# Kernel tuning notes

Measured on AMD Instinct MI355X. Metric: run time of the kernel, lower is better.

The kernel has to match this reference:

```python
import jax, jax.numpy as jnp
import numpy as np

D_MODEL = 1024
N_HEADS = 16
N_GROUPS = 4
HEAD_DIM = D_MODEL // N_HEADS          # 64
HPG = N_HEADS // N_GROUPS              # heads per group = 4
KV_DIM = N_GROUPS * HEAD_DIM           # 256


def setup_inputs() -> dict:
    key = jax.random.key(0)
    ks = jax.random.split(key, 9)
    B, T = 2, 2048
    s = 0.02
    return {
        "x":  jax.random.normal(ks[0], (B, T, D_MODEL), dtype=jnp.float32),
        "Wq": jax.random.normal(ks[1], (D_MODEL, D_MODEL), dtype=jnp.float32) * s,
        "bq": jnp.zeros((D_MODEL,), dtype=jnp.float32),
        "Wk": jax.random.normal(ks[2], (D_MODEL, KV_DIM), dtype=jnp.float32) * s,
        "bk": jnp.zeros((KV_DIM,), dtype=jnp.float32),
        "Wv": jax.random.normal(ks[3], (D_MODEL, KV_DIM), dtype=jnp.float32) * s,
        "bv": jnp.zeros((KV_DIM,), dtype=jnp.float32),
        "Wo": jax.random.normal(ks[4], (D_MODEL, D_MODEL), dtype=jnp.float32) * s,
        "bo": jnp.zeros((D_MODEL,), dtype=jnp.float32),
    }


def reference(x, Wq, bq, Wk, bk, Wv, bv, Wo, bo):
    B, T, C = x.shape
    q = x @ Wq + bq                                   # [B,T,C]
    k = x @ Wk + bk                                   # [B,T,G*hd]
    v = x @ Wv + bv

    # [B, G, hpg, T, hd] for q; [B, G, T, hd] for k,v (native GQA head sharing,
    # equivalent to repeat_interleave on the group dim in the torch code)
    q = q.reshape(B, T, N_GROUPS, HPG, HEAD_DIM).transpose(0, 2, 3, 1, 4)
    k = k.reshape(B, T, N_GROUPS, HEAD_DIM).transpose(0, 2, 1, 3)
    v = v.reshape(B, T, N_GROUPS, HEAD_DIM).transpose(0, 2, 1, 3)

    scale = 1.0 / jnp.sqrt(jnp.float32(HEAD_DIM))
    attn = jnp.einsum('bghqd,bgkd->bghqk', q, k) * scale   # [B,G,hpg,T,T]

    causal = jnp.tril(jnp.ones((T, T), dtype=bool))        # True = keep
    attn = jnp.where(causal, attn, jnp.float32(-jnp.inf))
    attn = jax.nn.softmax(attn, axis=-1)
    # dropout p=0.1 only in training mode; reference is eval mode (identity)

    out = jnp.einsum('bghqk,bgkd->bghqd', attn, v)         # [B,G,hpg,T,hd]
    out = out.transpose(0, 3, 1, 2, 4).reshape(B, T, C)
    return out @ Wo + bo
```

## Files before the change

### kernel.cpp

```cpp
#include <hip/hip_runtime.h>
#include <hip/hip_bf16.h>
#include <stdint.h>

#define D_MODEL 1024
#define T_LEN   2048
#define BATCH   2
#define N_HEADS 16
#define KV_DIM  256
#define QKV_N   1536
#define M_ROWS  (BATCH * T_LEN)

typedef unsigned short u16;
typedef __bf16 bf16x8 __attribute__((ext_vector_type(8)));
typedef __bf16 bf16x2 __attribute__((ext_vector_type(2)));
typedef float  f32x4  __attribute__((ext_vector_type(4)));

__device__ __forceinline__ u16 f2b(float f) {
    uint32_t u = __builtin_bit_cast(uint32_t, f);
    u += 0x7FFFu + ((u >> 16) & 1u);
    return (u16)(u >> 16);
}

__device__ __forceinline__ uint32_t pk_bf16(float a, float b) {
#if __has_builtin(__builtin_amdgcn_cvt_pk_bf16_f32)
    bf16x2 v = __builtin_amdgcn_cvt_pk_bf16_f32(a, b);
    return __builtin_bit_cast(uint32_t, v);
#else
    return (uint32_t)f2b(a) | ((uint32_t)f2b(b) << 16);
#endif
}

__device__ __forceinline__ void gl_lds16(const void* g, void* l) {
    __builtin_amdgcn_global_load_lds(g, l, 16, 0, 0);
}

__global__ __launch_bounds__(256) void prep(
    const float* __restrict__ x,
    const float* __restrict__ Wq, const float* __restrict__ Wk,
    const float* __restrict__ Wv, const float* __restrict__ Wo,
    u16* __restrict__ xb, u16* __restrict__ WcatT, u16* __restrict__ WoT)
{
    __shared__ u16 tile[32][33];
    int id = blockIdx.x;
    int tid = threadIdx.x;
    if (id < 2048) {
        int i = (id * 256 + tid) * 8;
        float4 a = *(const float4*)&x[i];
        float4 c = *(const float4*)&x[i + 4];
        u16 r[8] = { f2b(a.x), f2b(a.y), f2b(a.z), f2b(a.w),
                     f2b(c.x), f2b(c.y), f2b(c.z), f2b(c.w) };
        *(uint4*)&xb[i] = *(const uint4*)r;
        return;
    }
    int t = id - 2048;
    int bx = t % 80;
    int k0 = (t / 80) * 32;
    const float* src; u16* dst; int N, n0;
    if (bx < 32)       { src = Wq; dst = WcatT;                   N = 1024; n0 = bx * 32; }
    else if (bx < 40)  { src = Wk; dst = WcatT + 1024 * 1024;     N = 256;  n0 = (bx - 32) * 32; }
    else if (bx < 48)  { src = Wv; dst = WcatT + 1280 * 1024;     N = 256;  n0 = (bx - 40) * 32; }
    else               { src = Wo; dst = WoT;                     N = 1024; n0 = (bx - 48) * 32; }
    for (int i = 0; i < 4; ++i) {
        int idx = tid + i * 256;
        int r = idx >> 5, c = idx & 31;
        tile[r][c] = f2b(src[(size_t)(k0 + r) * N + (n0 + c)]);
    }
    __syncthreads();
    for (int i = 0; i < 4; ++i) {
        int idx = tid + i * 256;
        int r = idx >> 5, c = idx & 31;
        dst[(size_t)(n0 + r) * 1024 + (k0 + c)] = tile[c][r];
    }
}

__global__ __launch_bounds__(256) void gemm_qkv(
    const u16* __restrict__ A, const u16* __restrict__ BT,
    const float* __restrict__ bq, const float* __restrict__ bk,
    const float* __restrict__ bv, u16* __restrict__ Qb,
    u16* __restrict__ Kpack, u16* __restrict__ Vpack)
{
    constexpr int K = 1024;
    constexpr float SCALE = 0.125f * 1.44269504088896f;
    __shared__ __align__(16) u16 As[128 * 64];
    __shared__ __align__(16) u16 Bs[128 * 64];

    int tid  = threadIdx.x;
    int lane = tid & 63, w = tid >> 6;
    int quad = lane >> 4, l15 = lane & 15;
    int wr = w >> 1, wc = w & 1;
    int m0 = blockIdx.y * 128, n0 = blockIdx.x * 128;
    int lr = lane >> 3, lc = (lane & 7) * 8;

    f32x4 acc[4][4] = {};

    for (int k0 = 0; k0 < K; k0 += 64) {
        for (int t = 0; t < 4; ++t) {
            int rb = t * 32 + w * 8;
            gl_lds16(&A[(size_t)(m0 + rb + lr) * K + k0 + lc], &As[rb * 64]);
            gl_lds16(&BT[(size_t)(n0 + rb + lr) * K + k0 + lc], &Bs[rb * 64]);
        }
        __syncthreads();
        for (int kk = 0; kk < 64; kk += 32) {
            bf16x8 a[4], b[4];
            for (int i = 0; i < 4; ++i)
                a[i] = *(const bf16x8*)&As[(wr * 64 + i * 16 + l15) * 64 + kk + quad * 8];
            for (int j = 0; j < 4; ++j)
                b[j] = *(const bf16x8*)&Bs[(wc * 64 + j * 16 + l15) * 64 + kk + quad * 8];
            for (int i = 0; i < 4; ++i)
                for (int j = 0; j < 4; ++j)
                    acc[i][j] = __builtin_amdgcn_mfma_f32_16x16x32_bf16(
                        a[i], b[j], acc[i][j], 0, 0, 0);
        }
        __syncthreads();
    }

    for (int j = 0; j < 4; ++j) {
        int col = n0 + wc * 64 + j * 16 + l15;
        float bj = (col < 1024) ? bq[col] : (col < 1280) ? bk[col - 1024] : bv[col - 1280];
        for (int i = 0; i < 4; ++i) {
            int rowb = m0 + wr * 64 + i * 16 + quad * 4;
            int bb = rowb >> 11, keyloc = rowb & 2047;
            int t64 = keyloc >> 6;
            if (col < 1024) {
                for (int r = 0; r < 4; ++r)
                    Qb[(size_t)(rowb + r) * 1024 + col] =
                        f2b((acc[i][j][r] + bj) * SCALE);
            } else if (col < 1280) {
                int d = col - 1024; int g = d >> 6; d &= 63;
                int kk = d >> 5, qd = (d >> 3) & 3, e = d & 7;
                int ntk = (keyloc >> 4) & 3, l15k = keyloc & 15;
                size_t base = ((((size_t)(bb * 4 + g) * 32 + t64) * 2 + kk) * 4
                               + ntk) * 512 + qd * 128 + l15k * 8 + e;
                for (int r = 0; r < 4; ++r)
                    Kpack[base + r * 8] = f2b(acc[i][j][r] + bj);
            } else {
                int d = col - 1280; int g = d >> 6; d &= 63;
                int dt = d >> 4, l15v = d & 15;
                int kkp = (keyloc >> 5) & 1, qv = (keyloc >> 3) & 3, e0 = keyloc & 7;
                u16 tmp[4];
                for (int r = 0; r < 4; ++r) tmp[r] = f2b(acc[i][j][r] + bj);
                size_t base = ((((size_t)(bb * 4 + g) * 32 + t64) * 2 + kkp) * 4
                               + dt) * 512 + (qv * 16 + l15v) * 8 + e0;
                *(uint64_t*)&Vpack[base] = *(const uint64_t*)tmp;
            }
        }
    }
}

__global__ __launch_bounds__(256) void gemm_out(
    const u16* __restrict__ A, const u16* __restrict__ BT,
    const float* __restrict__ bias, float* __restrict__ C)
{
    constexpr int K = 1024, N = 1024;
    __shared__ __align__(16) u16 As[128 * 64];
    __shared__ __align__(16) u16 Bs[128 * 64];

    int tid  = threadIdx.x;
    int lane = tid & 63, w = tid >> 6;
    int quad = lane >> 4, l15 = lane & 15;
    int wr = w >> 1, wc = w & 1;
    int m0 = blockIdx.y * 128, n0 = blockIdx.x * 128;
    int lr = lane >> 3, lc = (lane & 7) * 8;

    f32x4 acc[4][4] = {};

    for (int k0 = 0; k0 < K; k0 += 64) {
        for (int t = 0; t < 4; ++t) {
            int rb = t * 32 + w * 8;
            gl_lds16(&A[(size_t)(m0 + rb + lr) * K + k0 + lc], &As[rb * 64]);
            gl_lds16(&BT[(size_t)(n0 + rb + lr) * K + k0 + lc], &Bs[rb * 64]);
        }
        __syncthreads();
        for (int kk = 0; kk < 64; kk += 32) {
            bf16x8 a[4], b[4];
            for (int i = 0; i < 4; ++i)
                a[i] = *(const bf16x8*)&As[(wr * 64 + i * 16 + l15) * 64 + kk + quad * 8];
            for (int j = 0; j < 4; ++j)
                b[j] = *(const bf16x8*)&Bs[(wc * 64 + j * 16 + l15) * 64 + kk + quad * 8];
            for (int i = 0; i < 4; ++i)
                for (int j = 0; j < 4; ++j)
                    acc[i][j] = __builtin_amdgcn_mfma_f32_16x16x32_bf16(
                        a[i], b[j], acc[i][j], 0, 0, 0);
        }
        __syncthreads();
    }

    for (int j = 0; j < 4; ++j) {
        int col = n0 + wc * 64 + j * 16 + l15;
        float bj = bias[col];
        for (int i = 0; i < 4; ++i) {
            int rowb = m0 + wr * 64 + i * 16 + quad * 4;
            for (int r = 0; r < 4; ++r)
                C[(size_t)(rowb + r) * N + col] = acc[i][j][r] + bj;
        }
    }
}

__global__ __launch_bounds__(256, 4) void attn_kernel(
    const u16* __restrict__ Qb,
    const u16* __restrict__ Kpack,
    const u16* __restrict__ Vpack,
    u16* __restrict__ AO)
{
    constexpr int LDP = 72;
    __shared__ __align__(16) u16 Ps[4][16 * LDP];

    int tid  = threadIdx.x;
    int lane = tid & 63, w = tid >> 6;
    int quad = lane >> 4, l15 = lane & 15;

    int gid = blockIdx.x;
    int b = gid & 1, g = (gid >> 1) & 3;
    int s = gid >> 3;
    int kq = s >> 5, tq = s & 31;
    int q4 = (kq & 1) ? tq : (31 - tq);
    int j  = q4 * 4 + kq;
    int head = g * 4 + w;
    int q0 = j * 16;
    int iters = q4 + 1;

    const u16* Qp = Qb + ((size_t)b * T_LEN + q0) * 1024 + head * 64;
    const u16* Kp = Kpack + (size_t)(b * 4 + g) * 131072 + (size_t)lane * 8;
    const u16* Vp = Vpack + (size_t)(b * 4 + g) * 131072 + (size_t)lane * 8;
    u16*       Op = AO + ((size_t)b * T_LEN + q0) * D_MODEL + head * 64;
    u16* Pw = Ps[w];

    bf16x8 Qfrag[2];
    #pragma unroll
    for (int kk = 0; kk < 2; ++kk)
        Qfrag[kk] = *(const bf16x8*)&Qp[(size_t)l15 * 1024 + kk * 32 + quad * 8];

    f32x4 o[4] = {};
    float lsum = 0.f;

    for (int tg = 0; tg < iters; ++tg) {
        bool diag = (tg == iters - 1);

        const u16* kb = Kp + (size_t)tg * 4096;
        bf16x8 aK[2][4];
        #pragma unroll
        for (int kk = 0; kk < 2; ++kk)
            #pragma unroll
            for (int ntk = 0; ntk < 4; ++ntk)
                aK[kk][ntk] = *(const bf16x8*)(kb + (kk * 4 + ntk) * 512);

        f32x4 sacc[4] = {};
        #pragma unroll
        for (int kk = 0; kk < 2; ++kk) {
            bf16x8 bQ = Qfrag[kk];
            #pragma unroll
            for (int ntk = 0; ntk < 4; ++ntk)
                sacc[ntk] = __builtin_amdgcn_mfma_f32_16x16x32_bf16(
                    aK[kk][ntk], bQ, sacc[ntk], 0, 0, 0);
        }
        int qrow = q0 + l15;
        float lacc = 0.f;
        #pragma unroll
        for (int ntk = 0; ntk < 4; ++ntk) {
            float p0, p1, p2, p3;
            if (diag) {
                int key = tg * 64 + ntk * 16 + quad * 4;
                p0 = (key + 0 <= qrow) ? exp2f(sacc[ntk][0]) : 0.f;
                p1 = (key + 1 <= qrow) ? exp2f(sacc[ntk][1]) : 0.f;
                p2 = (key + 2 <= qrow) ? exp2f(sacc[ntk][2]) : 0.f;
                p3 = (key + 3 <= qrow) ? exp2f(sacc[ntk][3]) : 0.f;
            } else {
                p0 = exp2f(sacc[ntk][0]);
                p1 = exp2f(sacc[ntk][1]);
                p2 = exp2f(sacc[ntk][2]);
                p3 = exp2f(sacc[ntk][3]);
            }
            lacc += (p0 + p1) + (p2 + p3);
            uint2 pv;
            pv.x = pk_bf16(p0, p1);
            pv.y = pk_bf16(p2, p3);
            *(uint2*)&Pw[l15 * LDP + ntk * 16 + quad * 4] = pv;
        }
        lsum += lacc;

        const u16* vb = Vp + (size_t)tg * 4096;
        #pragma unroll
        for (int kkp = 0; kkp < 2; ++kkp) {
            bf16x8 bV[4];
            #pragma unroll
            for (int dt = 0; dt < 4; ++dt)
                bV[dt] = *(const bf16x8*)(vb + (kkp * 4 + dt) * 512);
            bf16x8 aP = *(const bf16x8*)&Pw[l15 * LDP + kkp * 32 + quad * 8];
            #pragma unroll
            for (int dt = 0; dt < 4; ++dt)
                o[dt] = __builtin_amdgcn_mfma_f32_16x16x32_bf16(
                    aP, bV[dt], o[dt], 0, 0, 0);
        }
    }

    float l = lsum;
    l += __shfl_xor(l, 16, 64);
    l += __shfl_xor(l, 32, 64);
    float linv = 1.0f / l;
    float li[4];
    #pragma unroll
    for (int r = 0; r < 4; ++r)
        li[r] = __shfl(linv, quad * 4 + r, 64);
    #pragma unroll
    for (int dt = 0; dt < 4; ++dt)
        #pragma unroll
        for (int r = 0; r < 4; ++r)
            Op[(size_t)(quad * 4 + r) * D_MODEL + dt * 16 + l15] =
                f2b(o[dt][r] * li[r]);
}

extern "C" void kernel_launch(void* const* d_in, const int* in_sizes, int n_in,
                              void* d_out, int out_size, void* d_ws, size_t ws_size,
                              hipStream_t stream) {
    const float* x  = (const float*)d_in[0];
    const float* Wq = (const float*)d_in[1];
    const float* bq = (const float*)d_in[2];
    const float* Wk = (const float*)d_in[3];
    const float* bk = (const float*)d_in[4];
    const float* Wv = (const float*)d_in[5];
    const float* bv = (const float*)d_in[6];
    const float* Wo = (const float*)d_in[7];
    const float* bo = (const float*)d_in[8];
    float* out = (float*)d_out;

    u16* ws    = (u16*)d_ws;
    u16* xb    = ws;  ws += (size_t)M_ROWS * 1024;
    u16* WcatT = ws;  ws += (size_t)QKV_N * 1024;
    u16* WoT   = ws;  ws += 1024 * 1024;
    u16* Qb    = ws;  ws += (size_t)M_ROWS * 1024;
    u16* Kpack = ws;  ws += (size_t)M_ROWS * KV_DIM;
    u16* Vpack = ws;  ws += (size_t)M_ROWS * KV_DIM;
    u16* AO    = xb;

    prep<<<2048 + 2560, 256, 0, stream>>>(x, Wq, Wk, Wv, Wo, xb, WcatT, WoT);
    gemm_qkv<<<dim3(QKV_N / 128, M_ROWS / 128), 256, 0, stream>>>(
        xb, WcatT, bq, bk, bv, Qb, Kpack, Vpack);
    attn_kernel<<<1024, 256, 0, stream>>>(Qb, Kpack, Vpack, AO);
    gemm_out<<<dim3(1024 / 128, M_ROWS / 128), 256, 0, stream>>>(AO, WoT, bo, out);
}
```

Measured before the change: 194.4 us.

## Split attention KV range across two wave halves and shrink GEMM M tiles

The attention kernel now launches 512 threads per block. Two sets of four waves each process half of the key tiles for the same query block, and their partial outputs and row sums are merged through shared memory before normalisation. Both GEMMs switch to 64x128 tiles, which doubles the number of blocks so the 256 CUs are better filled. The attention merge adds LDS traffic and a block barrier. The smaller GEMM tiles lower per-block data reuse. The attention change looks sound only if the unseen loop body uses no running-max rescaling; otherwise the halves need a max combine.

Result: slower. 203.6 us (+4.7%).

```diff
diff --git a/kernel.cpp b/kernel.cpp
--- a/kernel.cpp
+++ b/kernel.cpp
@@ -81,44 +81,46 @@
 {
     constexpr int K = 1024;
     constexpr float SCALE = 0.125f * 1.44269504088896f;
-    __shared__ __align__(16) u16 As[128 * 64];
+    __shared__ __align__(16) u16 As[64 * 64];
     __shared__ __align__(16) u16 Bs[128 * 64];
 
     int tid  = threadIdx.x;
     int lane = tid & 63, w = tid >> 6;
     int quad = lane >> 4, l15 = lane & 15;
-    int wr = w >> 1, wc = w & 1;
-    int m0 = blockIdx.y * 128, n0 = blockIdx.x * 128;
+    int m0 = blockIdx.y * 64, n0 = blockIdx.x * 128;
     int lr = lane >> 3, lc = (lane & 7) * 8;
 
-    f32x4 acc[4][4] = {};
+    f32x4 acc[4][2] = {};
 
     for (int k0 = 0; k0 < K; k0 += 64) {
+        for (int t = 0; t < 2; ++t) {
+            int rb = t * 32 + w * 8;
+            gl_lds16(&A[(size_t)(m0 + rb + lr) * K + k0 + lc], &As[rb * 64]);
+        }
         for (int t = 0; t < 4; ++t) {
             int rb = t * 32 + w * 8;
-            gl_lds16(&A[(size_t)(m0 + rb + lr) * K + k0 + lc], &As[rb * 64]);
             gl_lds16(&BT[(size_t)(n0 + rb + lr) * K + k0 + lc], &Bs[rb * 64]);
         }
         __syncthreads();
         for (int kk = 0; kk < 64; kk += 32) {
-            bf16x8 a[4], b[4];
+            bf16x8 a[4], b[2];
             for (int i = 0; i < 4; ++i)
-                a[i] = *(const bf16x8*)&As[(wr * 64 + i * 16 + l15) * 64 + kk + quad * 8];
-            for (int j = 0; j < 4; ++j)
-                b[j] = *(const bf16x8*)&Bs[(wc * 64 + j * 16 + l15) * 64 + kk + quad * 8];
+                a[i] = *(const bf16x8*)&As[(i * 16 + l15) * 64 + kk + quad * 8];
+            for (int j = 0; j < 2; ++j)
+                b[j] = *(const bf16x8*)&Bs[(w * 32 + j * 16 + l15) * 64 + kk + quad * 8];
             for (int i = 0; i < 4; ++i)
-                for (int j = 0; j < 4; ++j)
+                for (int j = 0; j < 2; ++j)
                     acc[i][j] = __builtin_amdgcn_mfma_f32_16x16x32_bf16(
                         a[i], b[j], acc[i][j], 0, 0, 0);
         }
         __syncthreads();
     }
 
-    for (int j = 0; j < 4; ++j) {
-        int col = n0 + wc * 64 + j * 16 + l15;
+    for (int j = 0; j < 2; ++j) {
+        int col = n0 + w * 32 + j * 16 + l15;
         float bj = (col < 1024) ? bq[col] : (col < 1280) ? bk[col - 1024] : bv[col - 1280];
         for (int i = 0; i < 4; ++i) {
-            int rowb = m0 + wr * 64 + i * 16 + quad * 4;
+            int rowb = m0 + i * 16 + quad * 4;
             int bb = rowb >> 11, keyloc = rowb & 2047;
             int t64 = keyloc >> 6;
             if (col < 1024) {
@@ -152,62 +154,67 @@
     const float* __restrict__ bias, float* __restrict__ C)
 {
     constexpr int K = 1024, N = 1024;
-    __shared__ __align__(16) u16 As[128 * 64];
+    __shared__ __align__(16) u16 As[64 * 64];
     __shared__ __align__(16) u16 Bs[128 * 64];
 
     int tid  = threadIdx.x;
     int lane = tid & 63, w = tid >> 6;
     int quad = lane >> 4, l15 = lane & 15;
-    int wr = w >> 1, wc = w & 1;
-    int m0 = blockIdx.y * 128, n0 = blockIdx.x * 128;
+    int m0 = blockIdx.y * 64, n0 = blockIdx.x * 128;
     int lr = lane >> 3, lc = (lane & 7) * 8;
 
-    f32x4 acc[4][4] = {};
+    f32x4 acc[4][2] = {};
 
     for (int k0 = 0; k0 < K; k0 += 64) {
+        for (int t = 0; t < 2; ++t) {
+            int rb = t * 32 + w * 8;
+            gl_lds16(&A[(size_t)(m0 + rb + lr) * K + k0 + lc], &As[rb * 64]);
+        }
         for (int t = 0; t < 4; ++t) {
             int rb = t * 32 + w * 8;
-            gl_lds16(&A[(size_t)(m0 + rb + lr) * K + k0 + lc], &As[rb * 64]);
             gl_lds16(&BT[(size_t)(n0 + rb + lr) * K + k0 + lc], &Bs[rb * 64]);
         }
         __syncthreads();
         for (int kk = 0; kk < 64; kk += 32) {
-            bf16x8 a[4], b[4];
+            bf16x8 a[4], b[2];
             for (int i = 0; i < 4; ++i)
-                a[i] = *(const bf16x8*)&As[(wr * 64 + i * 16 + l15) * 64 + kk + quad * 8];
-            for (int j = 0; j < 4; ++j)
-                b[j] = *(const bf16x8*)&Bs[(wc * 64 + j * 16 + l15) * 64 + kk + quad * 8];
+                a[i] = *(const bf16x8*)&As[(i * 16 + l15) * 64 + kk + quad * 8];
+            for (int j = 0; j < 2; ++j)
+                b[j] = *(const bf16x8*)&Bs[(w * 32 + j * 16 + l15) * 64 + kk + quad * 8];
             for (int i = 0; i < 4; ++i)
-                for (int j = 0; j < 4; ++j)
+                for (int j = 0; j < 2; ++j)
                     acc[i][j] = __builtin_amdgcn_mfma_f32_16x16x32_bf16(
                         a[i], b[j], acc[i][j], 0, 0, 0);
         }
         __syncthreads();
     }
 
-    for (int j = 0; j < 4; ++j) {
-        int col = n0 + wc * 64 + j * 16 + l15;
+    for (int j = 0; j < 2; ++j) {
+        int col = n0 + w * 32 + j * 16 + l15;
         float bj = bias[col];
         for (int i = 0; i < 4; ++i) {
-            int rowb = m0 + wr * 64 + i * 16 + quad * 4;
+            int rowb = m0 + i * 16 + quad * 4;
             for (int r = 0; r < 4; ++r)
                 C[(size_t)(rowb + r) * N + col] = acc[i][j][r] + bj;
         }
     }
 }
 
-__global__ __launch_bounds__(256, 4) void attn_kernel(
+__global__ __launch_bounds__(512, 8) void attn_kernel(
     const u16* __restrict__ Qb,
     const u16* __restrict__ Kpack,
     const u16* __restrict__ Vpack,
     u16* __restrict__ AO)
 {
     constexpr int LDP = 72;
-    __shared__ __align__(16) u16 Ps[4][16 * LDP];
+    __shared__ __align__(16) u16 Ps[8][16 * LDP];
+    __shared__ __align__(16) float Co[4][64][16];
+    __shared__ float Cl[4][64];
 
     int tid  = threadIdx.x;
     int lane = tid & 63, w = tid >> 6;
     int quad = lane >> 4, l15 = lane & 15;
+    int hw = w & 3, half = w >> 2;
 
     int gid = blockIdx.x;
     int b = gid & 1, g = (gid >> 1) & 3;
@@ -215,9 +222,12 @@
     int kq = s >> 5, tq = s & 31;
     int q4 = (kq & 1) ? tq : (31 - tq);
     int j  = q4 * 4 + kq;
-    int head = g * 4 + w;
+    int head = g * 4 + hw;
     int q0 = j * 16;
     int iters = q4 + 1;
+    int n0 = (iters + 1) >> 1;
+    int tgB = half ? n0 : 0;
+    int tgE = half ? iters : n0;
 
     const u16* Qp = Qb + ((size_t)b * T_LEN + q0) * 1024 + head * 64;
     const u16* Kp = Kpack + (size_t)(b * 4 + g) * 131072 + (size_t)lane * 8;
@@ -233,7 +243,7 @@
     f32x4 o[4] = {};
     float lsum = 0.f;
 
-    for (int tg = 0; tg < iters; ++tg) {
+    for (int tg = tgB; tg < tgE; ++tg) {
         bool diag = (tg == iters - 1);
 
         const u16* kb = Kp + (size_t)tg * 4096;
@@ -293,20 +303,36 @@
         }
     }
 
-    float l = lsum;
-    l += __shfl_xor(l, 16, 64);
-    l += __shfl_xor(l, 32, 64);
-    float linv = 1.0f / l;
-    float li[4];
-    #pragma unroll
-    for (int r = 0; r < 4; ++r)
-        li[r] = __shfl(linv, quad * 4 + r, 64);
-    #pragma unroll
-    for (int dt = 0; dt < 4; ++dt)
+    if (half) {
+        #pragma unroll
+        for (int dt = 0; dt < 4; ++dt)
+            *(f32x4*)&Co[hw][lane][dt * 4] = o[dt];
+        Cl[hw][lane] = lsum;
+    }
+    __syncthreads();
+    if (!half) {
+        #pragma unroll
+        for (int dt = 0; dt < 4; ++dt) {
+            f32x4 t = *(const f32x4*)&Co[hw][lane][dt * 4];
+            o[dt] += t;
+        }
+        lsum += Cl[hw][lane];
+
+        float l = lsum;
+        l += __shfl_xor(l, 16, 64);
+        l += __shfl_xor(l, 32, 64);
+        float linv = 1.0f / l;
+        float li[4];
         #pragma unroll
         for (int r = 0; r < 4; ++r)
-            Op[(size_t)(quad * 4 + r) * D_MODEL + dt * 16 + l15] =
-                f2b(o[dt][r] * li[r]);
+            li[r] = __shfl(linv, quad * 4 + r, 64);
+        #pragma unroll
+        for (int dt = 0; dt < 4; ++dt)
+            #pragma unroll
+            for (int r = 0; r < 4; ++r)
+                Op[(size_t)(quad * 4 + r) * D_MODEL + dt * 16 + l15] =
+                    f2b(o[dt][r] * li[r]);
+    }
 }
 
 extern "C" void kernel_launch(void* const* d_in, const int* in_sizes, int n_in,
@@ -333,8 +359,8 @@
     u16* AO    = xb;
 
     prep<<<2048 + 2560, 256, 0, stream>>>(x, Wq, Wk, Wv, Wo, xb, WcatT, WoT);
-    gemm_qkv<<<dim3(QKV_N / 128, M_ROWS / 128), 256, 0, stream>>>(
+    gemm_qkv<<<dim3(QKV_N / 128, M_ROWS / 64), 256, 0, stream>>>(
         xb, WcatT, bq, bk, bv, Qb, Kpack, Vpack);
-    attn_kernel<<<1024, 256, 0, stream>>>(Qb, Kpack, Vpack, AO);
-    gemm_out<<<dim3(1024 / 128, M_ROWS / 128), 256, 0, stream>>>(AO, WoT, bo, out);
-}
+    attn_kernel<<<1024, 512, 0, stream>>>(Qb, Kpack, Vpack, AO);
+    gemm_out<<<dim3(1024 / 128, M_ROWS / 64), 256, 0, stream>>>(AO, WoT, bo, out);
+}
```
